# Optimization experiments

Hardware: AMD Instinct MI355X
Metric: run time of the kernel (lower is better)

Reference implementation:

```python
import jax, jax.numpy as jnp
import numpy as np

DIM = 512
HEADS = 8

def setup_inputs() -> dict:
    key = jax.random.key(0)
    ks = jax.random.split(key, 24)
    B, Nq, N3, N4, D = 8, 4096, 1024, 256, DIM
    def lin(k):
        k1, k2 = jax.random.split(k)
        s = 1.0 / np.sqrt(D)
        return (jax.random.uniform(k1, (D, D), jnp.float32, -s, s),
                jax.random.uniform(k2, (D,), jnp.float32, -s, s))
    Wq1, bq1 = lin(ks[0]); Wk1, bk1 = lin(ks[1]); Wv1, bv1 = lin(ks[2])
    Wq2, bq2 = lin(ks[3]); Wk2, bk2 = lin(ks[4]); Wv2, bv2 = lin(ks[5])
    sr = 1.0 / np.sqrt(2 * D)
    Wr = jax.random.uniform(ks[6], (D, 2 * D), jnp.float32, -sr, sr)
    br = jax.random.uniform(ks[7], (D,), jnp.float32, -sr, sr)
    return {
        'f2': jax.random.normal(ks[8], (B, Nq, D), jnp.float32),
        'f3': jax.random.normal(ks[9], (B, N3, D), jnp.float32),
        'f4': jax.random.normal(ks[10], (B, N4, D), jnp.float32),
        'f2_pos_embed': jax.random.normal(ks[11], (B, Nq, D), jnp.float32),
        'f3_pos_embed': jax.random.normal(ks[12], (B, N3, D), jnp.float32),
        'f4_pos_embed': jax.random.normal(ks[13], (B, N4, D), jnp.float32),
        'Wq1': Wq1, 'bq1': bq1, 'Wk1': Wk1, 'bk1': bk1, 'Wv1': Wv1, 'bv1': bv1,
        'Wq2': Wq2, 'bq2': bq2, 'Wk2': Wk2, 'bk2': bk2, 'Wv2': Wv2, 'bv2': bv2,
        'Wr': Wr, 'br': br,
    }

def _linear(x, W, b):
    return x @ W.T + b

def _efficient_branch(q, k, v, H):
    # q: [B,Nq,D], k/v: [B,Nk,D]. Split D into H heads of dh channels (contiguous).
    B, Nq, D = q.shape
    Nk = k.shape[1]
    dh = D // H
    q = q.reshape(B, Nq, H, dh)
    k = k.reshape(B, Nk, H, dh)
    v = v.reshape(B, Nk, H, dh)
    qs = jax.nn.softmax(q, axis=1)   # softmax over query positions (torch dim=2 in [B,C,N])
    ks = jax.nn.softmax(k, axis=3)   # softmax over head key channels (torch dim=1)
    # context[b,h,d,e] = sum_n ks[b,n,h,d] * v[b,n,h,e]  -> [B,H,dh,dh]
    context = jnp.einsum('bnhd,bnhe->bhde', ks, v)
    # attended[b,n,h,e] = sum_d context[b,h,d,e] * qs[b,n,h,d]
    attended = jnp.einsum('bhde,bnhd->bnhe', context, qs)
    return attended.reshape(B, Nq, D)

def reference(f2, f3, f4, f2_pos_embed, f3_pos_embed, f4_pos_embed,
              Wq1, bq1, Wk1, bk1, Wv1, bv1,
              Wq2, bq2, Wk2, bk2, Wv2, bv2, Wr, br):
    f2p = f2 + f2_pos_embed
    q1 = _linear(f2p, Wq1, bq1)
    q2 = _linear(f2p, Wq2, bq2)
    k3 = _linear(f3 + f3_pos_embed, Wk1, bk1)
    v3 = _linear(f3, Wv1, bv1)
    k4 = _linear(f4 + f4_pos_embed, Wk2, bk2)
    v4 = _linear(f4, Wv2, bv2)
    agg32 = _efficient_branch(q1, k3, v3, HEADS)  # [B,Nq,D]
    agg42 = _efficient_branch(q2, k4, v4, HEADS)  # [B,Nq,D]
    out = jnp.concatenate([agg32, agg42], axis=-1)
    return _linear(out, Wr, br)  # dropout p=0 -> identity
```

## Files before the change

kernel.cpp:

```cpp
#include <hip/hip_runtime.h>

typedef unsigned short ushort_t;
typedef unsigned int uint32;
typedef __attribute__((ext_vector_type(8))) short short8;
typedef __attribute__((ext_vector_type(4))) float f32x4;

static __device__ __forceinline__ ushort_t f2bf(float f) {
  uint32 u = __builtin_bit_cast(uint32, f);
  u += 0x7fffu + ((u >> 16) & 1u);
  return (ushort_t)(u >> 16);
}

static __device__ __forceinline__ void gload_lds16(const ushort_t* g, ushort_t* l) {
  __builtin_amdgcn_global_load_lds(
      (const __attribute__((address_space(1))) uint32*)g,
      (__attribute__((address_space(3))) uint32*)l, 16, 0, 0);
}

static __device__ __forceinline__ void addcvt4(const float* __restrict__ a,
                                               const float* __restrict__ b,
                                               ushort_t* __restrict__ o, int i) {
  float4 va = reinterpret_cast<const float4*>(a)[i];
  if (b != nullptr) {
    float4 vb = reinterpret_cast<const float4*>(b)[i];
    va.x += vb.x; va.y += vb.y; va.z += vb.z; va.w += vb.w;
  }
  ushort4 u;
  u.x = f2bf(va.x); u.y = f2bf(va.y); u.z = f2bf(va.z); u.w = f2bf(va.w);
  reinterpret_cast<ushort4*>(o)[i] = u;
}

__global__ void prepA_kernel(const float* __restrict__ f3, const float* __restrict__ f3pe,
                             const float* __restrict__ f4, const float* __restrict__ f4pe,
                             const float* __restrict__ Wq1, const float* __restrict__ Wq2,
                             const float* __restrict__ Wk1, const float* __restrict__ Wv1,
                             const float* __restrict__ Wk2, const float* __restrict__ Wv2,
                             const float* __restrict__ bq1, const float* __restrict__ bq2,
                             ushort_t* __restrict__ f3p, ushort_t* __restrict__ f3b,
                             ushort_t* __restrict__ f4p, ushort_t* __restrict__ f4b,
                             ushort_t* __restrict__ WqB, ushort_t* __restrict__ Wk1B,
                             ushort_t* __restrict__ Wv1B, ushort_t* __restrict__ Wk2B,
                             ushort_t* __restrict__ Wv2B, float* __restrict__ bqc,
                             float* __restrict__ Z, float* __restrict__ ctx) {
  int b = blockIdx.x, t = threadIdx.x;
  if (b < 4096) {
    int i = b * 256 + t;
    float4 va = reinterpret_cast<const float4*>(f3)[i];
    float4 vp = reinterpret_cast<const float4*>(f3pe)[i];
    ushort4 ub, up;
    ub.x = f2bf(va.x); ub.y = f2bf(va.y); ub.z = f2bf(va.z); ub.w = f2bf(va.w);
    up.x = f2bf(va.x + vp.x); up.y = f2bf(va.y + vp.y);
    up.z = f2bf(va.z + vp.z); up.w = f2bf(va.w + vp.w);
    reinterpret_cast<ushort4*>(f3b)[i] = ub;
    reinterpret_cast<ushort4*>(f3p)[i] = up;
  } else if (b < 5120) {
    int i = (b - 4096) * 256 + t;
    float4 va = reinterpret_cast<const float4*>(f4)[i];
    float4 vp = reinterpret_cast<const float4*>(f4pe)[i];
    ushort4 ub, up;
    ub.x = f2bf(va.x); ub.y = f2bf(va.y); ub.z = f2bf(va.z); ub.w = f2bf(va.w);
    up.x = f2bf(va.x + vp.x); up.y = f2bf(va.y + vp.y);
    up.z = f2bf(va.z + vp.z); up.w = f2bf(va.w + vp.w);
    reinterpret_cast<ushort4*>(f4b)[i] = ub;
    reinterpret_cast<ushort4*>(f4p)[i] = up;
  } else if (b < 6656) {
    int u = b - 5120;
    int arr = u >> 8, i = (u & 255) * 256 + t;
    const float* s; ushort_t* d;
    switch (arr) {
      case 0: s = Wq1; d = WqB; break;
      case 1: s = Wq2; d = WqB + 262144; break;
      case 2: s = Wk1; d = Wk1B; break;
      case 3: s = Wv1; d = Wv1B; break;
      case 4: s = Wk2; d = Wk2B; break;
      default: s = Wv2; d = Wv2B; break;
    }
    addcvt4(s, nullptr, d, i);
  } else if (b < 7168) {
    reinterpret_cast<float4*>(ctx)[(b - 6656) * 256 + t] = make_float4(0.f, 0.f, 0.f, 0.f);
  } else {
    for (int i = t; i < 512; i += 256) { bqc[i] = bq1[i]; bqc[512 + i] = bq2[i]; }
    for (int i = t; i < 8192; i += 256) Z[i] = 0.f;
  }
}

__global__ __launch_bounds__(256)
void ctxprepB_kernel(const ushort_t* __restrict__ ks3, const ushort_t* __restrict__ v3,
                     const ushort_t* __restrict__ ks4, const ushort_t* __restrict__ v4,
                     float* __restrict__ ctxOut,
                     const float* __restrict__ f2, const float* __restrict__ f2pe,
                     ushort_t* __restrict__ f2p) {
  __shared__ float ks_s[64][68];
  __shared__ float v_s[64][68];
  const int b = blockIdx.x, t = threadIdx.x;

  if (b >= 320) {
    const float4* A4 = reinterpret_cast<const float4*>(f2);
    const float4* P4 = reinterpret_cast<const float4*>(f2pe);
    uint4* O4 = reinterpret_cast<uint4*>(f2p);
    const int base = (b - 320) * 1024;
#pragma unroll
    for (int j = 0; j < 4; j++) {
      int i = base + j * 256 + t;
      float4 va = A4[i];
      float4 vp = P4[i];
      ushort4 u;
      u.x = f2bf(va.x + vp.x); u.y = f2bf(va.y + vp.y);
      u.z = f2bf(va.z + vp.z); u.w = f2bf(va.w + vp.w);
      reinterpret_cast<ushort4*>(O4)[i] = u;
    }
    return;
  }

  const ushort_t* ks; const ushort_t* v; float* dstBase; int Nk, bh, chunk;
  if (b < 256) { ks = ks3; v = v3; dstBase = ctxOut;          Nk = 1024; bh = b >> 2; chunk = b & 3; }
  else         { ks = ks4; v = v4; dstBase = ctxOut + 262144; Nk = 256;  bh = b - 256; chunk = 0; }
  const int bb = bh >> 3, h = bh & 7;
  const int td = t & 15, te = t >> 4;
  float acc[4][4] = {};
  size_t rowBase = (size_t)bb * Nk + chunk * 256;
  for (int n0 = 0; n0 < 256; n0 += 64) {
#pragma unroll
    for (int i = 0; i < 16; i++) {
      int idx = i * 256 + t;
      int n = idx >> 6, d = idx & 63;
      size_t g = (rowBase + n0 + n) * 512 + h * 64 + d;
      ks_s[n][d] = __builtin_bit_cast(float, (uint32)ks[g] << 16);
      v_s[n][d] = __builtin_bit_cast(float, (uint32)v[g] << 16);
    }
    __syncthreads();
#pragma unroll 8
    for (int n = 0; n < 64; n++) {
      float4 cv = *reinterpret_cast<const float4*>(&ks_s[n][td * 4]);
      float4 vv = *reinterpret_cast<const float4*>(&v_s[n][te * 4]);
      float ca[4] = {cv.x, cv.y, cv.z, cv.w};
      float va[4] = {vv.x, vv.y, vv.z, vv.w};
#pragma unroll
      for (int i = 0; i < 4; i++)
#pragma unroll
        for (int j = 0; j < 4; j++) acc[i][j] += ca[i] * va[j];
    }
    __syncthreads();
  }
  float* dst = dstBase + (size_t)bh * 4096;
#pragma unroll
  for (int i = 0; i < 4; i++)
#pragma unroll
    for (int j = 0; j < 4; j++)
      atomicAdd(&dst[(td * 4 + i) * 64 + te * 4 + j], acc[i][j]);
}

static __device__ __forceinline__ void gemm_core(
    const ushort_t* __restrict__ A, const ushort_t* __restrict__ Bt,
    int K, int mBase, int nBase, ushort_t* As, ushort_t* Bs, f32x4 acc[4][4]) {
  const int t = threadIdx.x;
  const int w = t >> 6, l = t & 63;
  const int l15 = l & 15, l4 = l >> 4;
  const int rowInSeg = l >> 3;
  const int srcOff = ((l & 7) ^ rowInSeg) << 3;
  const int wm = (w >> 1) * 64, wn = (w & 1) * 64;

  for (int k0 = 0; k0 < K; k0 += 64) {
#pragma unroll
    for (int i = 0; i < 4; i++) {
      int seg = w * 4 + i;
      int row = seg * 8 + rowInSeg;
      gload_lds16(A + (size_t)(mBase + row) * K + k0 + srcOff, As + seg * 512);
      gload_lds16(Bt + (size_t)(nBase + row) * K + k0 + srcOff, Bs + seg * 512);
    }
    __syncthreads();
#pragma unroll
    for (int kk = 0; kk < 2; kk++) {
      short8 af[4], bfr[4];
      const int kb = kk * 64 + l4 * 16;
#pragma unroll
      for (int f = 0; f < 4; f++) {
        int rowA = wm + f * 16 + l15;
        af[f] = *reinterpret_cast<const short8*>(
            reinterpret_cast<const char*>(As) + rowA * 128 + (kb ^ ((rowA & 7) << 4)));
        int rowB = wn + f * 16 + l15;
        bfr[f] = *reinterpret_cast<const short8*>(
            reinterpret_cast<const char*>(Bs) + rowB * 128 + (kb ^ ((rowB & 7) << 4)));
      }
#pragma unroll
      for (int fm = 0; fm < 4; fm++)
#pragma unroll
        for (int fn = 0; fn < 4; fn++)
          acc[fm][fn] = __builtin_amdgcn_mfma_f32_16x16x32_bf16(af[fm], bfr[fn], acc[fm][fn], 0, 0, 0);
    }
    __syncthreads();
  }
}

__global__ __launch_bounds__(256, 4)
void gemm_g1(const ushort_t* __restrict__ A, const ushort_t* __restrict__ Bt,
             const float* __restrict__ bias, ushort_t* __restrict__ E,
             float* __restrict__ Z) {
  __shared__ ushort_t As[8192], Bs[8192];
  const int bid = blockIdx.x;
  const int swz = (bid & 7) * 256 + (bid >> 3);
  const int mBase = (swz >> 3) * 128, nBase = (swz & 7) * 128;
  const int t = threadIdx.x, w = t >> 6, lane = t & 63;
  const int l15 = lane & 15, l4 = lane >> 4;
  const int wm = (w >> 1) * 64, wn = (w & 1) * 64;

  f32x4 acc[4][4];
#pragma unroll
  for (int i = 0; i < 4; i++)
#pragma unroll
    for (int j = 0; j < 4; j++) acc[i][j] = (f32x4){0.f, 0.f, 0.f, 0.f};

  gemm_core(A, Bt, 512, mBase, nBase, As, Bs, acc);

  const int N = 1024;
  float bcol[4], csum[4] = {0.f, 0.f, 0.f, 0.f};
#pragma unroll
  for (int fn = 0; fn < 4; fn++) bcol[fn] = bias[nBase + wn + fn * 16 + l15];
#pragma unroll
  for (int fm = 0; fm < 4; fm++) {
#pragma unroll
    for (int r = 0; r < 4; r++) {
      int row = mBase + wm + fm * 16 + l4 * 4 + r;
      float ex[4];
#pragma unroll
      for (int fn = 0; fn < 4; fn++) {
        ex[fn] = __expf(acc[fm][fn][r] + bcol[fn]);
        csum[fn] += ex[fn];
      }
#pragma unroll
      for (int fn = 0; fn < 4; fn++)
        E[(size_t)row * N + nBase + wn + fn * 16 + l15] = f2bf(ex[fn]);
    }
  }
#pragma unroll
  for (int fn = 0; fn < 4; fn++) {
    float s = csum[fn];
    s += __shfl_xor(s, 16);
    s += __shfl_xor(s, 32);
    if (l4 == 0) atomicAdd(&Z[(mBase >> 12) * 1024 + nBase + wn + fn * 16 + l15], s);
  }
}

__global__ __launch_bounds__(256, 4)
void kv_quad(const ushort_t* __restrict__ f3p, const ushort_t* __restrict__ f3b,
             const ushort_t* __restrict__ f4p, const ushort_t* __restrict__ f4b,
             const ushort_t* __restrict__ Wk1B, const ushort_t* __restrict__ Wv1B,
             const ushort_t* __restrict__ Wk2B, const ushort_t* __restrict__ Wv2B,
             const float* __restrict__ bk1, const float* __restrict__ bv1,
             const float* __restrict__ bk2, const float* __restrict__ bv2,
             ushort_t* __restrict__ ks3, ushort_t* __restrict__ v3,
             ushort_t* __restrict__ ks4, ushort_t* __restrict__ v4) {
  __shared__ ushort_t As[8192], Bs[8192];
  const int bid = blockIdx.x;
  const int id = (bid & 7) * 80 + (bid >> 3);
  const ushort_t* A; const ushort_t* Bt; const float* bias; ushort_t* out;
  bool doSM; int loc;
  if (id < 256)      { A = f3p; Bt = Wk1B; bias = bk1; out = ks3; doSM = true;  loc = id; }
  else if (id < 512) { A = f3b; Bt = Wv1B; bias = bv1; out = v3;  doSM = false; loc = id - 256; }
  else if (id < 576) { A = f4p; Bt = Wk2B; bias = bk2; out = ks4; doSM = true;  loc = id - 512; }
  else               { A = f4b; Bt = Wv2B; bias = bv2; out = v4;  doSM = false; loc = id - 576; }
  const int nBase = (loc & 3) * 128, mBase = (loc >> 2) * 128;
  const int t = threadIdx.x, w = t >> 6, lane = t & 63;
  const int l15 = lane & 15, l4 = lane >> 4;
  const int wm = (w >> 1) * 64, wn = (w & 1) * 64;

  f32x4 acc[4][4];
#pragma unroll
  for (int i = 0; i < 4; i++)
#pragma unroll
    for (int j = 0; j < 4; j++) acc[i][j] = (f32x4){0.f, 0.f, 0.f, 0.f};

  gemm_core(A, Bt, 512, mBase, nBase, As, Bs, acc);

  const int N = 512;
  float bcol[4];
#pragma unroll
  for (int fn = 0; fn < 4; fn++) bcol[fn] = bias[nBase + wn + fn * 16 + l15];

  if (doSM) {
#pragma unroll
    for (int fm = 0; fm < 4; fm++) {
#pragma unroll
      for (int r = 0; r < 4; r++) {
        float x[4], m = -1e30f;
#pragma unroll
        for (int fn = 0; fn < 4; fn++) { x[fn] = acc[fm][fn][r] + bcol[fn]; m = fmaxf(m, x[fn]); }
        m = fmaxf(m, __shfl_xor(m, 1));
        m = fmaxf(m, __shfl_xor(m, 2));
        m = fmaxf(m, __shfl_xor(m, 4));
        m = fmaxf(m, __shfl_xor(m, 8));
        float s = 0.f;
#pragma unroll
        for (int fn = 0; fn < 4; fn++) { x[fn] = __expf(x[fn] - m); s += x[fn]; }
        s += __shfl_xor(s, 1);
        s += __shfl_xor(s, 2);
        s += __shfl_xor(s, 4);
        s += __shfl_xor(s, 8);
        float inv = 1.f / s;
        int row = mBase + wm + fm * 16 + l4 * 4 + r;
#pragma unroll
        for (int fn = 0; fn < 4; fn++)
          out[(size_t)row * N + nBase + wn + fn * 16 + l15] = f2bf(x[fn] * inv);
      }
    }
  } else {
#pragma unroll
    for (int fm = 0; fm < 4; fm++) {
#pragma unroll
      for (int r = 0; r < 4; r++) {
        int row = mBase + wm + fm * 16 + l4 * 4 + r;
#pragma unroll
        for (int fn = 0; fn < 4; fn++)
          out[(size_t)row * N + nBase + wn + fn * 16 + l15] =
              f2bf(acc[fm][fn][r] + bcol[fn]);
      }
    }
  }
}

__global__ __launch_bounds__(256, 4)
void gemm_g2(const ushort_t* __restrict__ E, const ushort_t* __restrict__ Mt,
             const float* __restrict__ bias, float* __restrict__ C) {
  __shared__ ushort_t As[8192], Bs[8192];
  const int bid = blockIdx.x;
  const int swz = (bid & 7) * 128 + (bid >> 3);
  const int tx = swz & 3, ty = swz >> 2;
  const int mBase = ty * 128, nBase = tx * 128;
  const ushort_t* Btb = Mt + (size_t)(ty >> 5) * 524288;
  const int t = threadIdx.x, w = t >> 6, lane = t & 63;
  const int l15 = lane & 15, l4 = lane >> 4;
  const int wm = (w >> 1) * 64, wn = (w & 1) * 64;

  f32x4 acc[4][4];
#pragma unroll
  for (int i = 0; i < 4; i++)
#pragma unroll
    for (int j = 0; j < 4; j++) acc[i][j] = (f32x4){0.f, 0.f, 0.f, 0.f};

  gemm_core(E, Btb, 1024, mBase, nBase, As, Bs, acc);

  const int N = 512;
  float bcol[4];
#pragma unroll
  for (int fn = 0; fn < 4; fn++) bcol[fn] = bias[nBase + wn + fn * 16 + l15];
#pragma unroll
  for (int fm = 0; fm < 4; fm++) {
#pragma unroll
    for (int r = 0; r < 4; r++) {
      int row = mBase + wm + fm * 16 + l4 * 4 + r;
#pragma unroll
      for (int fn = 0; fn < 4; fn++)
        C[(size_t)row * N + nBase + wn + fn * 16 + l15] = acc[fm][fn][r] + bcol[fn];
    }
  }
}

__global__ __launch_bounds__(256)
void fold_kernel(const float* __restrict__ ctx, const float* __restrict__ Wr,
                 const float* __restrict__ Z, ushort_t* __restrict__ Mt) {
  __shared__ float ctxT[64][68];
  __shared__ float wrT[64][68];
  __shared__ float zinv[64];
  int blk = blockIdx.x;
  int jc = blk & 7;
  int h = (blk >> 3) & 7;
  int branch = (blk >> 6) & 1;
  int b = blk >> 7;
  int t = threadIdx.x;
  int cbase = branch * 512 + h * 64;
  const float* csrc = ctx + (size_t)(branch * 64 + b * 8 + h) * 4096;
#pragma unroll
  for (int i = 0; i < 16; i++) {
    int idx = i * 256 + t;
    int d = idx >> 6, e = idx & 63;
    ctxT[e][d] = csrc[d * 64 + e];
  }
#pragma unroll
  for (int i = 0; i < 16; i++) {
    int idx = i * 256 + t;
    int jl = idx >> 6, e = idx & 63;
    wrT[e][jl] = Wr[(size_t)(jc * 64 + jl) * 1024 + cbase + e];
  }
  if (t < 64) zinv[t] = 1.0f / Z[b * 1024 + cbase + t];
  __syncthreads();
  int td = t & 15, tj = t >> 4;
  float acc[4][4] = {};
#pragma unroll 8
  for (int e = 0; e < 64; e++) {
    float4 cv = *reinterpret_cast<const float4*>(&ctxT[e][td * 4]);
    float4 wv = *reinterpret_cast<const float4*>(&wrT[e][tj * 4]);
    float ca[4] = {cv.x, cv.y, cv.z, cv.w};
    float wa[4] = {wv.x, wv.y, wv.z, wv.w};
#pragma unroll
    for (int i = 0; i < 4; i++)
#pragma unroll
      for (int jj = 0; jj < 4; jj++) acc[i][jj] += ca[i] * wa[jj];
  }
  float zi[4] = {zinv[td * 4], zinv[td * 4 + 1], zinv[td * 4 + 2], zinv[td * 4 + 3]};
#pragma unroll
  for (int jj = 0; jj < 4; jj++) {
    ushort4 u;
    u.x = f2bf(acc[0][jj] * zi[0]);
    u.y = f2bf(acc[1][jj] * zi[1]);
    u.z = f2bf(acc[2][jj] * zi[2]);
    u.w = f2bf(acc[3][jj] * zi[3]);
    *reinterpret_cast<ushort4*>(
        &Mt[(size_t)(b * 512 + jc * 64 + tj * 4 + jj) * 1024 + cbase + td * 4]) = u;
  }
}

extern "C" void kernel_launch(void* const* d_in, const int* in_sizes, int n_in,
                              void* d_out, int out_size, void* d_ws, size_t ws_size,
                              hipStream_t stream) {
  const float* f2 = (const float*)d_in[0];
  const float* f3 = (const float*)d_in[1];
  const float* f4 = (const float*)d_in[2];
  const float* f2pe = (const float*)d_in[3];
  const float* f3pe = (const float*)d_in[4];
  const float* f4pe = (const float*)d_in[5];
  const float* Wq1 = (const float*)d_in[6];
  const float* bq1 = (const float*)d_in[7];
  const float* Wk1 = (const float*)d_in[8];
  const float* bk1 = (const float*)d_in[9];
  const float* Wv1 = (const float*)d_in[10];
  const float* bv1 = (const float*)d_in[11];
  const float* Wq2 = (const float*)d_in[12];
  const float* bq2 = (const float*)d_in[13];
  const float* Wk2 = (const float*)d_in[14];
  const float* bk2 = (const float*)d_in[15];
  const float* Wv2 = (const float*)d_in[16];
  const float* bv2 = (const float*)d_in[17];
  const float* Wr = (const float*)d_in[18];
  const float* br = (const float*)d_in[19];

  char* ws = (char*)d_ws;
  ushort_t* E = (ushort_t*)(ws + 0);
  char* R1 = ws + 67108864;
  ushort_t* f3p = (ushort_t*)R1;
  ushort_t* f3b = (ushort_t*)(R1 + 8388608);
  ushort_t* f4p = (ushort_t*)(R1 + 16777216);
  ushort_t* f4b = (ushort_t*)(R1 + 18874368);
  ushort_t* f2p = (ushort_t*)R1;
  char* R2 = ws + 100663296;
  ushort_t* ks3 = (ushort_t*)R2;
  ushort_t* v3b = (ushort_t*)(R2 + 8388608);
  ushort_t* ks4 = (ushort_t*)(R2 + 16777216);
  ushort_t* v4b = (ushort_t*)(R2 + 18874368);
  char* R3 = ws + 121634816;
  ushort_t* WqB = (ushort_t*)R3;
  ushort_t* Wk1B = (ushort_t*)(R3 + 1048576);
  ushort_t* Wv1B = (ushort_t*)(R3 + 1572864);
  ushort_t* Wk2B = (ushort_t*)(R3 + 2097152);
  ushort_t* Wv2B = (ushort_t*)(R3 + 2621440);
  ushort_t* Mt = (ushort_t*)(R3 + 3145728);
  float* Z = (float*)(R3 + 11534336);
  float* bqc = (float*)(R3 + 11567104);
  float* ctx = (float*)(R3 + 11571200);

  prepA_kernel<<<7169, 256, 0, stream>>>(f3, f3pe, f4, f4pe,
                                         Wq1, Wq2, Wk1, Wv1, Wk2, Wv2, bq1, bq2,
                                         f3p, f3b, f4p, f4b,
                                         WqB, Wk1B, Wv1B, Wk2B, Wv2B, bqc, Z, ctx);

  kv_quad<<<640, 256, 0, stream>>>(f3p, f3b, f4p, f4b,
                                   Wk1B, Wv1B, Wk2B, Wv2B,
                                   bk1, bv1, bk2, bv2,
                                   ks3, v3b, ks4, v4b);

  ctxprepB_kernel<<<4416, 256, 0, stream>>>(ks3, v3b, ks4, v4b, ctx, f2, f2pe, f2p);

  gemm_g1<<<2048, 256, 0, stream>>>(f2p, WqB, bqc, E, Z);

  fold_kernel<<<1024, 256, 0, stream>>>(ctx, Wr, Z, Mt);

  gemm_g2<<<1024, 256, 0, stream>>>(E, Mt, br, (float*)d_out);
}
```

Measured before the change: 181.6 us.

## Fold ctx reduction into gemm_g1 and f2 prep into kv_quad, dropping a launch

When the workspace is large enough, f2p gets its own buffer, so the f2+pos-embed bf16 conversion moves into extra blocks of kv_quad and the K^T V context reduction moves into the first 320 blocks of gemm_g1. This removes the separate ctxprepB launch and lets these small stages run alongside larger GEMM work. The context kernel now keeps bf16 in LDS with vectorized ushort4 loads instead of scalar loads and float staging, halving its LDS footprint. The cost is extra workspace use and heterogeneous blocks inside the GEMM grid, which can hurt load balance.

```diff
diff --git a/kernel.cpp b/kernel.cpp
--- a/kernel.cpp
+++ b/kernel.cpp
@@ -9,6 +9,9 @@
   uint32 u = __builtin_bit_cast(uint32, f);
   u += 0x7fffu + ((u >> 16) & 1u);
   return (ushort_t)(u >> 16);
+}
+static __device__ __forceinline__ float bf2f(ushort_t h) {
+  return __builtin_bit_cast(float, (uint32)h << 16);
 }
 
 static __device__ __forceinline__ void gload_lds16(const ushort_t* g, ushort_t* l) {
@@ -28,6 +31,51 @@
   ushort4 u;
   u.x = f2bf(va.x); u.y = f2bf(va.y); u.z = f2bf(va.z); u.w = f2bf(va.w);
   reinterpret_cast<ushort4*>(o)[i] = u;
+}
+
+static __device__ __forceinline__ void ctx_block(
+    const ushort_t* __restrict__ ks3, const ushort_t* __restrict__ v3,
+    const ushort_t* __restrict__ ks4, const ushort_t* __restrict__ v4,
+    float* __restrict__ ctxOut, int cb, ushort_t* sm) {
+  ushort_t (*ks_s)[68] = reinterpret_cast<ushort_t(*)[68]>(sm);
+  ushort_t (*v_s)[68] = reinterpret_cast<ushort_t(*)[68]>(sm + 4352);
+  const int t = threadIdx.x;
+  const ushort_t* ks; const ushort_t* v; float* dstBase; int Nk, bh, chunk;
+  if (cb < 256) { ks = ks3; v = v3; dstBase = ctxOut;          Nk = 1024; bh = cb >> 2; chunk = cb & 3; }
+  else          { ks = ks4; v = v4; dstBase = ctxOut + 262144; Nk = 256;  bh = cb - 256; chunk = 0; }
+  const int bb = bh >> 3, h = bh & 7;
+  const int td = t & 15, te = t >> 4;
+  float acc[4][4] = {};
+  size_t rowBase = (size_t)bb * Nk + chunk * 256;
+  for (int n0 = 0; n0 < 256; n0 += 64) {
+#pragma unroll
+    for (int i = 0; i < 4; i++) {
+      int idx = i * 256 + t;
+      int n = idx >> 4, dq = idx & 15;
+      size_t g = (rowBase + n0 + n) * 512 + h * 64 + dq * 4;
+      *reinterpret_cast<ushort4*>(&ks_s[n][dq * 4]) = *reinterpret_cast<const ushort4*>(ks + g);
+      *reinterpret_cast<ushort4*>(&v_s[n][dq * 4]) = *reinterpret_cast<const ushort4*>(v + g);
+    }
+    __syncthreads();
+#pragma unroll 8
+    for (int n = 0; n < 64; n++) {
+      ushort4 cu = *reinterpret_cast<const ushort4*>(&ks_s[n][td * 4]);
+      ushort4 vu = *reinterpret_cast<const ushort4*>(&v_s[n][te * 4]);
+      float ca[4] = {bf2f(cu.x), bf2f(cu.y), bf2f(cu.z), bf2f(cu.w)};
+      float va[4] = {bf2f(vu.x), bf2f(vu.y), bf2f(vu.z), bf2f(vu.w)};
+#pragma unroll
+      for (int i = 0; i < 4; i++)
+#pragma unroll
+        for (int j = 0; j < 4; j++) acc[i][j] += ca[i] * va[j];
+    }
+    __syncthreads();
+  }
+  float* dst = dstBase + (size_t)bh * 4096;
+#pragma unroll
+  for (int i = 0; i < 4; i++)
+#pragma unroll
+    for (int j = 0; j < 4; j++)
+      atomicAdd(&dst[(td * 4 + i) * 64 + te * 4 + j], acc[i][j]);
 }
 
 __global__ void prepA_kernel(const float* __restrict__ f3, const float* __restrict__ f3pe,
@@ -84,72 +132,6 @@
   }
 }
 
-__global__ __launch_bounds__(256)
-void ctxprepB_kernel(const ushort_t* __restrict__ ks3, const ushort_t* __restrict__ v3,
-                     const ushort_t* __restrict__ ks4, const ushort_t* __restrict__ v4,
-                     float* __restrict__ ctxOut,
-                     const float* __restrict__ f2, const float* __restrict__ f2pe,
-                     ushort_t* __restrict__ f2p) {
-  __shared__ float ks_s[64][68];
-  __shared__ float v_s[64][68];
-  const int b = blockIdx.x, t = threadIdx.x;
-
-  if (b >= 320) {
-    const float4* A4 = reinterpret_cast<const float4*>(f2);
-    const float4* P4 = reinterpret_cast<const float4*>(f2pe);
-    uint4* O4 = reinterpret_cast<uint4*>(f2p);
-    const int base = (b - 320) * 1024;
-#pragma unroll
-    for (int j = 0; j < 4; j++) {
-      int i = base + j * 256 + t;
-      float4 va = A4[i];
-      float4 vp = P4[i];
-      ushort4 u;
-      u.x = f2bf(va.x + vp.x); u.y = f2bf(va.y + vp.y);
-      u.z = f2bf(va.z + vp.z); u.w = f2bf(va.w + vp.w);
-      reinterpret_cast<ushort4*>(O4)[i] = u;
-    }
-    return;
-  }
-
-  const ushort_t* ks; const ushort_t* v; float* dstBase; int Nk, bh, chunk;
-  if (b < 256) { ks = ks3; v = v3; dstBase = ctxOut;          Nk = 1024; bh = b >> 2; chunk = b & 3; }
-  else         { ks = ks4; v = v4; dstBase = ctxOut + 262144; Nk = 256;  bh = b - 256; chunk = 0; }
-  const int bb = bh >> 3, h = bh & 7;
-  const int td = t & 15, te = t >> 4;
-  float acc[4][4] = {};
-  size_t rowBase = (size_t)bb * Nk + chunk * 256;
-  for (int n0 = 0; n0 < 256; n0 += 64) {
-#pragma unroll
-    for (int i = 0; i < 16; i++) {
-      int idx = i * 256 + t;
-      int n = idx >> 6, d = idx & 63;
-      size_t g = (rowBase + n0 + n) * 512 + h * 64 + d;
-      ks_s[n][d] = __builtin_bit_cast(float, (uint32)ks[g] << 16);
-      v_s[n][d] = __builtin_bit_cast(float, (uint32)v[g] << 16);
-    }
-    __syncthreads();
-#pragma unroll 8
-    for (int n = 0; n < 64; n++) {
-      float4 cv = *reinterpret_cast<const float4*>(&ks_s[n][td * 4]);
-      float4 vv = *reinterpret_cast<const float4*>(&v_s[n][te * 4]);
-      float ca[4] = {cv.x, cv.y, cv.z, cv.w};
-      float va[4] = {vv.x, vv.y, vv.z, vv.w};
-#pragma unroll
-      for (int i = 0; i < 4; i++)
-#pragma unroll
-        for (int j = 0; j < 4; j++) acc[i][j] += ca[i] * va[j];
-    }
-    __syncthreads();
-  }
-  float* dst = dstBase + (size_t)bh * 4096;
-#pragma unroll
-  for (int i = 0; i < 4; i++)
-#pragma unroll
-    for (int j = 0; j < 4; j++)
-      atomicAdd(&dst[(td * 4 + i) * 64 + te * 4 + j], acc[i][j]);
-}
-
 static __device__ __forceinline__ void gemm_core(
     const ushort_t* __restrict__ A, const ushort_t* __restrict__ Bt,
     int K, int mBase, int nBase, ushort_t* As, ushort_t* Bs, f32x4 acc[4][4]) {
@@ -195,9 +177,18 @@
 __global__ __launch_bounds__(256, 4)
 void gemm_g1(const ushort_t* __restrict__ A, const ushort_t* __restrict__ Bt,
              const float* __restrict__ bias, ushort_t* __restrict__ E,
-             float* __restrict__ Z) {
-  __shared__ ushort_t As[8192], Bs[8192];
-  const int bid = blockIdx.x;
+             float* __restrict__ Z,
+             const ushort_t* __restrict__ ks3, const ushort_t* __restrict__ v3,
+             const ushort_t* __restrict__ ks4, const ushort_t* __restrict__ v4,
+             float* __restrict__ ctx, int ctxBlocks) {
+  __shared__ ushort_t smem[16384];
+  if ((int)blockIdx.x < ctxBlocks) {
+    ctx_block(ks3, v3, ks4, v4, ctx, blockIdx.x, smem);
+    return;
+  }
+  ushort_t* As = smem;
+  ushort_t* Bs = smem + 8192;
+  const int bid = blockIdx.x - ctxBlocks;
   const int swz = (bid & 7) * 256 + (bid >> 3);
   const int mBase = (swz >> 3) * 128, nBase = (swz & 7) * 128;
   const int t = threadIdx.x, w = t >> 6, lane = t & 63;
@@ -249,9 +240,36 @@
              const float* __restrict__ bk1, const float* __restrict__ bv1,
              const float* __restrict__ bk2, const float* __restrict__ bv2,
              ushort_t* __restrict__ ks3, ushort_t* __restrict__ v3,
-             ushort_t* __restrict__ ks4, ushort_t* __restrict__ v4) {
+             ushort_t* __restrict__ ks4, ushort_t* __restrict__ v4,
+             const float* __restrict__ f2, const float* __restrict__ f2pe,
+             ushort_t* __restrict__ f2p) {
   __shared__ ushort_t As[8192], Bs[8192];
   const int bid = blockIdx.x;
+  if (bid >= 640) {
+    const int base = (bid - 640) * 2048;
+    const float4* A4 = reinterpret_cast<const float4*>(f2);
+    const float4* P4 = reinterpret_cast<const float4*>(f2pe);
+    const int t = threadIdx.x;
+#pragma unroll
+    for (int half = 0; half < 2; half++) {
+      float4 a[4], p[4];
+#pragma unroll
+      for (int j = 0; j < 4; j++) {
+        int i = base + (half * 4 + j) * 256 + t;
+        a[j] = A4[i];
+        p[j] = P4[i];
+      }
+#pragma unroll
+      for (int j = 0; j < 4; j++) {
+        int i = base + (half * 4 + j) * 256 + t;
+        ushort4 u;
+        u.x = f2bf(a[j].x + p[j].x); u.y = f2bf(a[j].y + p[j].y);
+        u.z = f2bf(a[j].z + p[j].z); u.w = f2bf(a[j].w + p[j].w);
+        reinterpret_cast<ushort4*>(f2p)[i] = u;
+      }
+    }
+    return;
+  }
   const int id = (bid & 7) * 80 + (bid >> 3);
   const ushort_t* A; const ushort_t* Bt; const float* bias; ushort_t* out;
   bool doSM; int loc;
@@ -316,6 +334,32 @@
       }
     }
   }
+}
+
+__global__ __launch_bounds__(256)
+void ctxprepB_kernel(const ushort_t* __restrict__ ks3, const ushort_t* __restrict__ v3,
+                     const ushort_t* __restrict__ ks4, const ushort_t* __restrict__ v4,
+                     float* __restrict__ ctxOut,
+                     const float* __restrict__ f2, const float* __restrict__ f2pe,
+                     ushort_t* __restrict__ f2p) {
+  __shared__ ushort_t sm[8704];
+  const int b = blockIdx.x, t = threadIdx.x;
+  if (b >= 320) {
+    const int base = (b - 320) * 1024;
+    const float4* A4 = reinterpret_cast<const float4*>(f2);
+    const float4* P4 = reinterpret_cast<const float4*>(f2pe);
+#pragma unroll
+    for (int j = 0; j < 4; j++) {
+      int i = base + j * 256 + t;
+      float4 a = A4[i], p = P4[i];
+      ushort4 u;
+      u.x = f2bf(a.x + p.x); u.y = f2bf(a.y + p.y);
+      u.z = f2bf(a.z + p.z); u.w = f2bf(a.w + p.w);
+      reinterpret_cast<ushort4*>(f2p)[i] = u;
+    }
+    return;
+  }
+  ctx_block(ks3, v3, ks4, v4, ctxOut, b, sm);
 }
 
 __global__ __launch_bounds__(256, 4)
@@ -440,7 +484,6 @@
   ushort_t* f3b = (ushort_t*)(R1 + 8388608);
   ushort_t* f4p = (ushort_t*)(R1 + 16777216);
   ushort_t* f4b = (ushort_t*)(R1 + 18874368);
-  ushort_t* f2p = (ushort_t*)R1;
   char* R2 = ws + 100663296;
   ushort_t* ks3 = (ushort_t*)R2;
   ushort_t* v3b = (ushort_t*)(R2 + 8388608);
@@ -456,20 +499,30 @@
   float* Z = (float*)(R3 + 11534336);
   float* bqc = (float*)(R3 + 11567104);
   float* ctx = (float*)(R3 + 11571200);
+  const bool bigWS = ws_size >= (size_t)176160768;
+  ushort_t* f2p = bigWS ? (ushort_t*)(ws + 142606336) : (ushort_t*)R1;
 
   prepA_kernel<<<7169, 256, 0, stream>>>(f3, f3pe, f4, f4pe,
                                          Wq1, Wq2, Wk1, Wv1, Wk2, Wv2, bq1, bq2,
                                          f3p, f3b, f4p, f4b,
                                          WqB, Wk1B, Wv1B, Wk2B, Wv2B, bqc, Z, ctx);
 
-  kv_quad<<<640, 256, 0, stream>>>(f3p, f3b, f4p, f4b,
-                                   Wk1B, Wv1B, Wk2B, Wv2B,
-                                   bk1, bv1, bk2, bv2,
-                                   ks3, v3b, ks4, v4b);
-
-  ctxprepB_kernel<<<4416, 256, 0, stream>>>(ks3, v3b, ks4, v4b, ctx, f2, f2pe, f2p);
-
-  gemm_g1<<<2048, 256, 0, stream>>>(f2p, WqB, bqc, E, Z);
+  if (bigWS) {
+    kv_quad<<<2688, 256, 0, stream>>>(f3p, f3b, f4p, f4b,
+                                      Wk1B, Wv1B, Wk2B, Wv2B,
+                                      bk1, bv1, bk2, bv2,
+                                      ks3, v3b, ks4, v4b, f2, f2pe, f2p);
+    gemm_g1<<<2368, 256, 0, stream>>>(f2p, WqB, bqc, E, Z,
+                                      ks3, v3b, ks4, v4b, ctx, 320);
+  } else {
+    kv_quad<<<640, 256, 0, stream>>>(f3p, f3b, f4p, f4b,
+                                     Wk1B, Wv1B, Wk2B, Wv2B,
+                                     bk1, bv1, bk2, bv2,
+                                     ks3, v3b, ks4, v4b, f2, f2pe, f2p);
+    ctxprepB_kernel<<<4416, 256, 0, stream>>>(ks3, v3b, ks4, v4b, ctx, f2, f2pe, f2p);
+    gemm_g1<<<2048, 256, 0, stream>>>(f2p, WqB, bqc, E, Z,
+                                      ks3, v3b, ks4, v4b, ctx, 0);
+  }
 
   fold_kernel<<<1024, 256, 0, stream>>>(ctx, Wr, Z, Mt);
 
```

New measurement: 175.6 us. 1.03x faster.
